# Optimization experiments

Measured on AMD Instinct MI355X. Metric: run time of the kernel, lower is better.

## Reference

```python
import jax, jax.numpy as jnp
import numpy as np

# dims
B, N, C_A, C_S, C_Z = 2, 8192, 128, 384, 16
H, D = 4, 32            # n_heads, head_dim (H*D == C_A)
NQ, NK = 32, 128        # local window: queries / keys
NB = 3                  # n_blocks
W = N // NQ             # number of query windows
HID = 2 * C_A           # transition expansion (n=2)


def _ln(x, eps=1e-5):
    # LayerNorm without affine params
    m = jnp.mean(x, axis=-1, keepdims=True)
    v = jnp.var(x, axis=-1, keepdims=True)
    return (x - m) * jax.lax.rsqrt(v + eps)


def setup_inputs() -> dict:
    key = jax.random.key(0)
    ks = iter(jax.random.split(key, 40))
    def rn(shape, scale=1.0):
        return jax.random.normal(next(ks), shape, dtype=jnp.float32) * jnp.float32(scale)
    inp = {
        'q': rn((B, N, C_A)),
        's': rn((B, N, C_S)),
        'p': rn((B, W, NQ, NK, C_Z)),
        # AttentionPairBias (AF3 Alg 24) params, stacked over blocks
        'adaln_scale_w': rn((NB, C_S, C_A), C_S ** -0.5),
        'adaln_scale_b': jnp.zeros((NB, C_A), jnp.float32),
        'adaln_shift_w': rn((NB, C_S, C_A), C_S ** -0.5),
        'wq': rn((NB, C_A, H * D), C_A ** -0.5),
        'bq': jnp.zeros((NB, H * D), jnp.float32),
        'wk': rn((NB, C_A, H * D), C_A ** -0.5),
        'wv': rn((NB, C_A, H * D), C_A ** -0.5),
        'lnz_w': jnp.ones((NB, C_Z), jnp.float32),
        'lnz_b': jnp.zeros((NB, C_Z), jnp.float32),
        'wb_pair': rn((NB, C_Z, H), C_Z ** -0.5),
        'wg': rn((NB, C_A, H * D), C_A ** -0.5),
        'wo': rn((NB, H * D, C_A), (H * D) ** -0.5),
        'sgate_w': rn((NB, C_S, C_A), C_S ** -0.5),
        'sgate_b': jnp.full((NB, C_A), -2.0, jnp.float32),
        # ConditionedTransitionBlock (AF3 Alg 25) params
        't_scale_w': rn((NB, C_S, C_A), C_S ** -0.5),
        't_scale_b': jnp.zeros((NB, C_A), jnp.float32),
        't_shift_w': rn((NB, C_S, C_A), C_S ** -0.5),
        't_wa': rn((NB, C_A, HID), C_A ** -0.5),
        't_wb': rn((NB, C_A, HID), C_A ** -0.5),
        't_wo': rn((NB, HID, C_A), HID ** -0.5),
        't_sgate_w': rn((NB, C_S, C_A), C_S ** -0.5),
        't_sgate_b': jnp.full((NB, C_A), -2.0, jnp.float32),
    }
    return inp


def reference(q, s, p,
              adaln_scale_w, adaln_scale_b, adaln_shift_w,
              wq, bq, wk, wv, lnz_w, lnz_b, wb_pair, wg, wo, sgate_w, sgate_b,
              t_scale_w, t_scale_b, t_shift_w, t_wa, t_wb, t_wo, t_sgate_w, t_sgate_b):
    a = q
    s_ln = _ln(s)  # [B, N, C_S], shared across blocks
    # local window key indices: window w covers queries [w*NQ, (w+1)*NQ), keys
    # are a centered NK-wide window -> offsets in [-(NK-NQ)//2, ...)
    off = (NK - NQ) // 2
    idx = jnp.arange(W)[:, None] * NQ - off + jnp.arange(NK)[None, :]  # [W, NK]
    valid = (idx >= 0) & (idx < N)
    idx_c = jnp.clip(idx, 0, N - 1)
    inv_sqrt_d = jnp.float32(1.0 / np.sqrt(D))
    NEG = jnp.float32(-1e9)

    for i in range(NB):
        # ---- AttentionPairBias (AdaLN-conditioned, pair-biased, gated) ----
        a_ln = _ln(a)
        a_ln = jax.nn.sigmoid(s_ln @ adaln_scale_w[i] + adaln_scale_b[i]) * a_ln \
               + s_ln @ adaln_shift_w[i]
        qh = (a_ln @ wq[i] + bq[i]).reshape(B, N, H, D)
        kh = (a_ln @ wk[i]).reshape(B, N, H, D)
        vh = (a_ln @ wv[i]).reshape(B, N, H, D)
        g = jax.nn.sigmoid(a_ln @ wg[i]).reshape(B, N, H, D)
        # pair bias from z: LN + linear to heads -> [B, W, NQ, NK, H]
        bias = (_ln(p) * lnz_w[i] + lnz_b[i]) @ wb_pair[i]
        qw = qh.reshape(B, W, NQ, H, D)
        kw = kh[:, idx_c]  # [B, W, NK, H, D]
        vw = vh[:, idx_c]
        logits = jnp.einsum('bwqhd,bwkhd->bwqkh', qw, kw) * inv_sqrt_d + bias
        logits = jnp.where(valid[None, :, None, :, None], logits, NEG)
        attn = jax.nn.softmax(logits, axis=3)
        ow = jnp.einsum('bwqkh,bwkhd->bwqhd', attn, vw)
        o = (g * ow.reshape(B, N, H, D)).reshape(B, N, H * D)
        attn_out = (o @ wo[i]) * jax.nn.sigmoid(s_ln @ sgate_w[i] + sgate_b[i])
        # ---- ConditionedTransitionBlock (SwiGLU, sigmoid-gated) ----
        t_ln = _ln(a)
        t_ln = jax.nn.sigmoid(s_ln @ t_scale_w[i] + t_scale_b[i]) * t_ln \
               + s_ln @ t_shift_w[i]
        hidden = jax.nn.silu(t_ln @ t_wa[i]) * (t_ln @ t_wb[i])
        trans_out = (hidden @ t_wo[i]) * jax.nn.sigmoid(s_ln @ t_sgate_w[i] + t_sgate_b[i])
        # AF3 Alg 23: a <- b + ConditionedTransitionBlock(a, s)
        a = attn_out + trans_out
    return a
```

## Files before the change

kernel.cpp:

```cpp
#include <hip/hip_runtime.h>
#include <hip/hip_bf16.h>
#include <cstddef>
#include <cstdint>

#define BB   2
#define NN   8192
#define CA   128
#define CS   384
#define CZ   16
#define HH   4
#define DD   32
#define NQW  32
#define NKW  128
#define NBLK 3
#define WW   256
#define MR   (BB*NN)
#define HIDN 256

typedef unsigned short u16;
typedef __attribute__((ext_vector_type(8))) short short8;
typedef __attribute__((ext_vector_type(4))) float floatx4;

__device__ __forceinline__ float sigmoidf_(float x) { return 1.f / (1.f + __expf(-x)); }

__device__ __forceinline__ u16 f2bf(float x) {
  unsigned u = __float_as_uint(x);
  unsigned r = (u + 0x7fffu + ((u >> 16) & 1u)) >> 16;
  return (u16)r;
}
__device__ __forceinline__ float bf2f(u16 u) {
  return __uint_as_float(((unsigned)u) << 16);
}

__global__ __launch_bounds__(256) void ln_s_kernel(const float* __restrict__ s,
                                                   u16* __restrict__ s_ln_bf) {
  int row  = blockIdx.x * 4 + (threadIdx.x >> 6);
  int lane = threadIdx.x & 63;
  const float* sr = s + (size_t)row * CS;
  float x[6];
  float sum = 0.f, sq = 0.f;
#pragma unroll
  for (int t = 0; t < 6; ++t) { x[t] = sr[lane + 64*t]; sum += x[t]; sq += x[t]*x[t]; }
#pragma unroll
  for (int off = 32; off; off >>= 1) { sum += __shfl_down(sum, off); sq += __shfl_down(sq, off); }
  sum = __shfl(sum, 0); sq = __shfl(sq, 0);
  float mean = sum * (1.f/CS);
  float var  = sq  * (1.f/CS) - mean*mean;
  float rstd = rsqrtf(var + 1e-5f);
  u16* orow = s_ln_bf + (size_t)row * CS;
#pragma unroll
  for (int t = 0; t < 6; ++t) orow[lane + 64*t] = f2bf((x[t]-mean)*rstd);
}

__global__ __launch_bounds__(256) void modln_kernel(const float* __restrict__ a,
                                                    const u16* __restrict__ sp0,
                                                    const u16* __restrict__ sp1,
                                                    const u16* __restrict__ sp3,
                                                    const u16* __restrict__ sp4,
                                                    u16* __restrict__ amod,
                                                    u16* __restrict__ tmod) {
  int row  = blockIdx.x * 4 + (threadIdx.x >> 6);
  int lane = threadIdx.x & 63;
  const float* ar = a + (size_t)row * CA;
  float x0 = ar[lane], x1 = ar[lane + 64];
  float sum = x0 + x1, sq = x0*x0 + x1*x1;
#pragma unroll
  for (int off = 32; off; off >>= 1) { sum += __shfl_down(sum, off); sq += __shfl_down(sq, off); }
  sum = __shfl(sum, 0); sq = __shfl(sq, 0);
  float mean = sum * (1.f/CA);
  float var  = sq  * (1.f/CA) - mean*mean;
  float rstd = rsqrtf(var + 1e-5f);
  float n0 = (x0-mean)*rstd, n1 = (x1-mean)*rstd;
  size_t i0 = (size_t)row * CA + lane;
  amod[i0]      = f2bf(bf2f(sp0[i0])     *n0 + bf2f(sp1[i0]));
  amod[i0 + 64] = f2bf(bf2f(sp0[i0 + 64])*n1 + bf2f(sp1[i0 + 64]));
  tmod[i0]      = f2bf(bf2f(sp3[i0])     *n0 + bf2f(sp4[i0]));
  tmod[i0 + 64] = f2bf(bf2f(sp3[i0 + 64])*n1 + bf2f(sp4[i0 + 64]));
}

struct TJob { const float* src; u16* dst; int K; int N; };
struct TJobs { TJob j[42]; };

__global__ __launch_bounds__(256) void transpose_bf16(TJobs jobs) {
  TJob jb = jobs.j[blockIdx.z];
  int tk = blockIdx.x * 32, tn = blockIdx.y * 32;
  if (tk >= jb.K || tn >= jb.N) return;
  __shared__ float tile[32][33];
  int tx = threadIdx.x & 31;
  int ty = threadIdx.x >> 5;
#pragma unroll
  for (int r = ty; r < 32; r += 8) tile[r][tx] = jb.src[(size_t)(tk + r) * jb.N + tn + tx];
  __syncthreads();
#pragma unroll
  for (int r = ty; r < 32; r += 8)
    jb.dst[(size_t)(tn + r) * jb.K + tk + tx] = f2bf(tile[tx][r]);
}

struct GemmJob {
  const u16* A;
  const u16* Bt;
  const u16* Bt2;
  const float* bias;
  u16* outbf;
  int K;
  int ostride;
  int mode;
  int pad;
};
struct GemmJobs { GemmJob j[18]; };

#define CH_STRIDE 1032

template <bool DUAL>
__global__ __launch_bounds__(256) void gemm_mfma(GemmJobs jobs) {
  GemmJob jb = jobs.j[blockIdx.z];
  const int bm = blockIdx.y * 128, bn = blockIdx.x * 128;
  const int K = jb.K;

  __shared__ u16 As[4 * CH_STRIDE];
  __shared__ u16 Bs[4 * CH_STRIDE];
  __shared__ u16 Bs2[DUAL ? 4 * CH_STRIDE : 8];

  const int tid  = threadIdx.x;
  const int lane = tid & 63;
  const int wave = tid >> 6;
  const int wr = wave >> 1, wc = wave & 1;
  const int l15 = lane & 15, quad = lane >> 4;

  floatx4 acc[4][4] = {};
  floatx4 acc2[DUAL ? 4 : 1][DUAL ? 4 : 1] = {};

  for (int k0 = 0; k0 < K; k0 += 32) {
    __syncthreads();
#pragma unroll
    for (int h = 0; h < 2; ++h) {
      int f = tid + 256 * h;
      int m = f >> 2, c = f & 3;
      uint4 av = *(const uint4*)(jb.A + (size_t)(bm + m) * K + k0 + c * 8);
      *(uint4*)(As + c * CH_STRIDE + m * 8) = av;
      uint4 bv = *(const uint4*)(jb.Bt + (size_t)(bn + m) * K + k0 + c * 8);
      *(uint4*)(Bs + c * CH_STRIDE + m * 8) = bv;
      if constexpr (DUAL) {
        uint4 bv2 = *(const uint4*)(jb.Bt2 + (size_t)(bn + m) * K + k0 + c * 8);
        *(uint4*)(Bs2 + c * CH_STRIDE + m * 8) = bv2;
      }
    }
    __syncthreads();

    short8 a_frag[4], b_frag[4];
#pragma unroll
    for (int mt = 0; mt < 4; ++mt)
      a_frag[mt] = *(const short8*)(As + quad * CH_STRIDE + (wr * 64 + mt * 16 + l15) * 8);
#pragma unroll
    for (int nt = 0; nt < 4; ++nt)
      b_frag[nt] = *(const short8*)(Bs + quad * CH_STRIDE + (wc * 64 + nt * 16 + l15) * 8);
#pragma unroll
    for (int mt = 0; mt < 4; ++mt)
#pragma unroll
      for (int nt = 0; nt < 4; ++nt)
        acc[mt][nt] = __builtin_amdgcn_mfma_f32_16x16x32_bf16(a_frag[mt], b_frag[nt], acc[mt][nt], 0, 0, 0);
    if constexpr (DUAL) {
      short8 b2_frag[4];
#pragma unroll
      for (int nt = 0; nt < 4; ++nt)
        b2_frag[nt] = *(const short8*)(Bs2 + quad * CH_STRIDE + (wc * 64 + nt * 16 + l15) * 8);
#pragma unroll
      for (int mt = 0; mt < 4; ++mt)
#pragma unroll
        for (int nt = 0; nt < 4; ++nt)
          acc2[mt][nt] = __builtin_amdgcn_mfma_f32_16x16x32_bf16(a_frag[mt], b2_frag[nt], acc2[mt][nt], 0, 0, 0);
    }
  }

#pragma unroll
  for (int mt = 0; mt < 4; ++mt) {
#pragma unroll
    for (int nt = 0; nt < 4; ++nt) {
      int n = bn + wc * 64 + nt * 16 + l15;
      int mbase = bm + wr * 64 + mt * 16 + quad * 4;
      floatx4 v = acc[mt][nt];
      if constexpr (DUAL) {
        floatx4 v2 = acc2[mt][nt];
#pragma unroll
        for (int r = 0; r < 4; ++r) {
          size_t idx = (size_t)(mbase + r) * jb.ostride + n;
          float x1 = v[r];
          jb.outbf[idx] = f2bf(x1 * sigmoidf_(x1) * v2[r]);
        }
      } else if (jb.mode == 5) {
        int bidx = mbase >> 13;
        int tok  = mbase & (NN - 1);
        ushort4 o;
        o.x = f2bf(v[0]); o.y = f2bf(v[1]); o.z = f2bf(v[2]); o.w = f2bf(v[3]);
        *(ushort4*)(jb.outbf + (size_t)(bidx * CA + n) * NN + tok) = o;
      } else {
        float bias = jb.bias ? jb.bias[n] : 0.f;
#pragma unroll
        for (int r = 0; r < 4; ++r) {
          size_t idx = (size_t)(mbase + r) * jb.ostride + n;
          float x = v[r] + bias;
          jb.outbf[idx] = f2bf(jb.mode == 1 ? sigmoidf_(x) : x);
        }
      }
    }
  }
}

__global__ __launch_bounds__(256) void combo_kernel(const u16* __restrict__ O,
                                                    const u16* __restrict__ HID,
                                                    const u16* __restrict__ woT,
                                                    const u16* __restrict__ twoT,
                                                    const u16* __restrict__ g1,
                                                    const u16* __restrict__ g2,
                                                    float* __restrict__ outp) {
  const int bm = blockIdx.y * 128;
  __shared__ u16 As[4 * CH_STRIDE];
  __shared__ u16 Bs[4 * CH_STRIDE];
  const int tid  = threadIdx.x;
  const int lane = tid & 63;
  const int wave = tid >> 6;
  const int wr = wave >> 1, wc = wave & 1;
  const int l15 = lane & 15, quad = lane >> 4;

  floatx4 acc1[4][4] = {};
  floatx4 acc2[4][4] = {};

  for (int k0 = 0; k0 < CA; k0 += 32) {
    __syncthreads();
#pragma unroll
    for (int h = 0; h < 2; ++h) {
      int f = tid + 256 * h;
      int m = f >> 2, c = f & 3;
      *(uint4*)(As + c * CH_STRIDE + m * 8) = *(const uint4*)(O + (size_t)(bm + m) * CA + k0 + c * 8);
      *(uint4*)(Bs + c * CH_STRIDE + m * 8) = *(const uint4*)(woT + (size_t)m * CA + k0 + c * 8);
    }
    __syncthreads();
    short8 a_frag[4], b_frag[4];
#pragma unroll
    for (int mt = 0; mt < 4; ++mt)
      a_frag[mt] = *(const short8*)(As + quad * CH_STRIDE + (wr * 64 + mt * 16 + l15) * 8);
#pragma unroll
    for (int nt = 0; nt < 4; ++nt)
      b_frag[nt] = *(const short8*)(Bs + quad * CH_STRIDE + (wc * 64 + nt * 16 + l15) * 8);
#pragma unroll
    for (int mt = 0; mt < 4; ++mt)
#pragma unroll
      for (int nt = 0; nt < 4; ++nt)
        acc1[mt][nt] = __builtin_amdgcn_mfma_f32_16x16x32_bf16(a_frag[mt], b_frag[nt], acc1[mt][nt], 0, 0, 0);
  }
  for (int k0 = 0; k0 < HIDN; k0 += 32) {
    __syncthreads();
#pragma unroll
    for (int h = 0; h < 2; ++h) {
      int f = tid + 256 * h;
      int m = f >> 2, c = f & 3;
      *(uint4*)(As + c * CH_STRIDE + m * 8) = *(const uint4*)(HID + (size_t)(bm + m) * HIDN + k0 + c * 8);
      *(uint4*)(Bs + c * CH_STRIDE + m * 8) = *(const uint4*)(twoT + (size_t)m * HIDN + k0 + c * 8);
    }
    __syncthreads();
    short8 a_frag[4], b_frag[4];
#pragma unroll
    for (int mt = 0; mt < 4; ++mt)
      a_frag[mt] = *(const short8*)(As + quad * CH_STRIDE + (wr * 64 + mt * 16 + l15) * 8);
#pragma unroll
    for (int nt = 0; nt < 4; ++nt)
      b_frag[nt] = *(const short8*)(Bs + quad * CH_STRIDE + (wc * 64 + nt * 16 + l15) * 8);
#pragma unroll
    for (int mt = 0; mt < 4; ++mt)
#pragma unroll
      for (int nt = 0; nt < 4; ++nt)
        acc2[mt][nt] = __builtin_amdgcn_mfma_f32_16x16x32_bf16(a_frag[mt], b_frag[nt], acc2[mt][nt], 0, 0, 0);
  }

#pragma unroll
  for (int mt = 0; mt < 4; ++mt) {
#pragma unroll
    for (int nt = 0; nt < 4; ++nt) {
      int n = wc * 64 + nt * 16 + l15;
      int mbase = bm + wr * 64 + mt * 16 + quad * 4;
#pragma unroll
      for (int r = 0; r < 4; ++r) {
        size_t idx = (size_t)(mbase + r) * CA + n;
        outp[idx] = acc1[mt][nt][r] * bf2f(g1[idx]) + acc2[mt][nt][r] * bf2f(g2[idx]);
      }
    }
  }
}

__global__ __launch_bounds__(256) void bias3_kernel(const float* __restrict__ p,
                                                    const float* __restrict__ lnz_w,
                                                    const float* __restrict__ lnz_b,
                                                    const float* __restrict__ wb,
                                                    u16* __restrict__ biasT) {
  const int kc = blockIdx.x, w = blockIdx.y, b = blockIdx.z;
  __shared__ float effW[12][16];
  __shared__ float effb[12];
  const int t = threadIdx.x;
  if (t < 192) {
    int i = t >> 6, rem = t & 63, z = rem >> 2, hh = rem & 3;
    effW[i*4 + hh][z] = lnz_w[i*CZ + z] * wb[(i*CZ + z)*HH + hh];
  }
  if (t < 12) {
    int i = t >> 2, hh = t & 3;
    float acc = 0.f;
    for (int z = 0; z < 16; ++z) acc += lnz_b[i*CZ + z] * wb[(i*CZ + z)*HH + hh];
    effb[t] = acc;
  }
  __syncthreads();

  const int kk = t & 31, qg = (t >> 5) * 4;
  const int k = kc * 32 + kk;
  u16 out4[12][4];
#pragma unroll
  for (int r = 0; r < 4; ++r) {
    int qq = qg + r;
    const float4* pr = (const float4*)(p + (size_t)(((b * WW + w) * NQW + qq) * NKW + k) * 16);
    float4 p0 = pr[0], p1 = pr[1], p2 = pr[2], p3 = pr[3];
    float x[16] = {p0.x,p0.y,p0.z,p0.w, p1.x,p1.y,p1.z,p1.w,
                   p2.x,p2.y,p2.z,p2.w, p3.x,p3.y,p3.z,p3.w};
    float sum = 0.f, sq = 0.f;
#pragma unroll
    for (int z = 0; z < 16; ++z) { sum += x[z]; sq += x[z]*x[z]; }
    float mean = sum * (1.f/16.f);
    float var  = sq  * (1.f/16.f) - mean*mean;
    float rstd = rsqrtf(var + 1e-5f);
#pragma unroll
    for (int ih = 0; ih < 12; ++ih) {
      float acc = effb[ih];
#pragma unroll
      for (int z = 0; z < 16; ++z) acc += (x[z]-mean)*rstd * effW[ih][z];
      out4[ih][r] = f2bf(acc);
    }
  }
#pragma unroll
  for (int ih = 0; ih < 12; ++ih) {
    int i = ih >> 2, hh = ih & 3;
    u16* dst = biasT + ((((size_t)i * BB + b) * WW + w) * HH + hh) * 4096 + (size_t)k * 32 + qg;
    ushort4 uv; uv.x = out4[ih][0]; uv.y = out4[ih][1]; uv.z = out4[ih][2]; uv.w = out4[ih][3];
    *(ushort4*)dst = uv;
  }
}

__global__ __launch_bounds__(64) void attn_mfma(const u16* __restrict__ Qb,
                                                const u16* __restrict__ Kb,
                                                const u16* __restrict__ Vtb,
                                                const u16* __restrict__ Gb,
                                                const u16* __restrict__ biasT,
                                                u16* __restrict__ Ob) {
  const int w = blockIdx.x, h = blockIdx.y, b = blockIdx.z;
  __shared__ u16 Pt[128 * 36];
  __shared__ float inv_s[32];
  const int lane = threadIdx.x;
  const int l15 = lane & 15, quad = lane >> 4;
  const int tok0 = w * NQW - 48;

  short8 qf[2];
#pragma unroll
  for (int mt = 0; mt < 2; ++mt) {
    int qq = w * NQW + mt * 16 + l15;
    qf[mt] = *(const short8*)(Qb + (size_t)(b * NN + qq) * CA + h * DD + quad * 8);
  }
  floatx4 lg[2][8] = {};
#pragma unroll
  for (int nt = 0; nt < 8; ++nt) {
    int tk = tok0 + nt * 16 + l15;
    int tc = min(max(tk, 0), NN - 1);
    short8 kf = *(const short8*)(Kb + (size_t)(b * NN + tc) * CA + h * DD + quad * 8);
#pragma unroll
    for (int mt = 0; mt < 2; ++mt)
      lg[mt][nt] = __builtin_amdgcn_mfma_f32_16x16x32_bf16(qf[mt], kf, lg[mt][nt], 0, 0, 0);
  }

  const float scale = 0.17677669529663687f;
  const u16* bb = biasT + ((((size_t)b * WW + w) * HH + h) << 12);
  float mrow[2][4];
#pragma unroll
  for (int mt = 0; mt < 2; ++mt)
#pragma unroll
    for (int r = 0; r < 4; ++r) mrow[mt][r] = -3.0e38f;
#pragma unroll
  for (int nt = 0; nt < 8; ++nt) {
    int tk = tok0 + nt * 16 + l15;
    bool valid = (tk >= 0) && (tk < NN);
#pragma unroll
    for (int mt = 0; mt < 2; ++mt) {
      ushort4 bv = *(const ushort4*)(bb + (nt * 16 + l15) * 32 + mt * 16 + quad * 4);
      float bvf[4] = {bf2f(bv.x), bf2f(bv.y), bf2f(bv.z), bf2f(bv.w)};
#pragma unroll
      for (int r = 0; r < 4; ++r) {
        float l = valid ? (lg[mt][nt][r] * scale + bvf[r]) : -1e9f;
        lg[mt][nt][r] = l;
        mrow[mt][r] = fmaxf(mrow[mt][r], l);
      }
    }
  }
#pragma unroll
  for (int mt = 0; mt < 2; ++mt)
#pragma unroll
    for (int r = 0; r < 4; ++r) {
      float m = mrow[mt][r];
      m = fmaxf(m, __shfl_xor(m, 1));
      m = fmaxf(m, __shfl_xor(m, 2));
      m = fmaxf(m, __shfl_xor(m, 4));
      m = fmaxf(m, __shfl_xor(m, 8));
      mrow[mt][r] = m;
    }

  float srow[2][4] = {};
#pragma unroll
  for (int nt = 0; nt < 8; ++nt)
#pragma unroll
    for (int mt = 0; mt < 2; ++mt) {
      u16 pv[4];
#pragma unroll
      for (int r = 0; r < 4; ++r) {
        float e = __expf(lg[mt][nt][r] - mrow[mt][r]);
        srow[mt][r] += e;
        pv[r] = f2bf(e);
      }
      ushort4 uv; uv.x = pv[0]; uv.y = pv[1]; uv.z = pv[2]; uv.w = pv[3];
      *(ushort4*)(Pt + (nt * 16 + l15) * 36 + mt * 16 + quad * 4) = uv;
    }
#pragma unroll
  for (int mt = 0; mt < 2; ++mt)
#pragma unroll
    for (int r = 0; r < 4; ++r) {
      float ssum = srow[mt][r];
      ssum += __shfl_xor(ssum, 1);
      ssum += __shfl_xor(ssum, 2);
      ssum += __shfl_xor(ssum, 4);
      ssum += __shfl_xor(ssum, 8);
      if (l15 == 0) inv_s[mt * 16 + quad * 4 + r] = 1.f / ssum;
    }
  __syncthreads();

  floatx4 oacc[2][2] = {};
#pragma unroll
  for (int ks = 0; ks < 4; ++ks) {
    short8 pf[2];
#pragma unroll
    for (int ntq = 0; ntq < 2; ++ntq)
#pragma unroll
      for (int j = 0; j < 8; ++j)
        pf[ntq][j] = (short)Pt[(ks * 32 + quad * 8 + j) * 36 + ntq * 16 + l15];
    int tb = tok0 + ks * 32 + quad * 8;
    tb = min(max(tb, 0), NN - 8);
#pragma unroll
    for (int mtd = 0; mtd < 2; ++mtd) {
      short8 vf = *(const short8*)(Vtb + (size_t)(b * CA + h * DD + mtd * 16 + l15) * NN + tb);
#pragma unroll
      for (int ntq = 0; ntq < 2; ++ntq)
        oacc[mtd][ntq] = __builtin_amdgcn_mfma_f32_16x16x32_bf16(vf, pf[ntq], oacc[mtd][ntq], 0, 0, 0);
    }
  }

#pragma unroll
  for (int mtd = 0; mtd < 2; ++mtd)
#pragma unroll
    for (int ntq = 0; ntq < 2; ++ntq) {
      int qq = ntq * 16 + l15;
      float inv = inv_s[qq];
      int tok = w * NQW + qq;
      size_t base = (size_t)(b * NN + tok) * CA + h * DD + mtd * 16 + quad * 4;
      ushort4 gv = *(const ushort4*)(Gb + base);
      floatx4 v = oacc[mtd][ntq];
      ushort4 o;
      o.x = f2bf(bf2f(gv.x) * v[0] * inv);
      o.y = f2bf(bf2f(gv.y) * v[1] * inv);
      o.z = f2bf(bf2f(gv.z) * v[2] * inv);
      o.w = f2bf(bf2f(gv.w) * v[3] * inv);
      *(ushort4*)(Ob + base) = o;
    }
}

extern "C" void kernel_launch(void* const* d_in, const int* in_sizes, int n_in,
                              void* d_out, int out_size, void* d_ws, size_t ws_size,
                              hipStream_t stream) {
  const float* q             = (const float*)d_in[0];
  const float* s             = (const float*)d_in[1];
  const float* p             = (const float*)d_in[2];
  const float* adaln_scale_w = (const float*)d_in[3];
  const float* adaln_scale_b = (const float*)d_in[4];
  const float* adaln_shift_w = (const float*)d_in[5];
  const float* wq            = (const float*)d_in[6];
  const float* bq            = (const float*)d_in[7];
  const float* wk            = (const float*)d_in[8];
  const float* wv            = (const float*)d_in[9];
  const float* lnz_w         = (const float*)d_in[10];
  const float* lnz_b         = (const float*)d_in[11];
  const float* wb_pair       = (const float*)d_in[12];
  const float* wg            = (const float*)d_in[13];
  const float* wo            = (const float*)d_in[14];
  const float* sgate_w       = (const float*)d_in[15];
  const float* sgate_b       = (const float*)d_in[16];
  const float* t_scale_w     = (const float*)d_in[17];
  const float* t_scale_b     = (const float*)d_in[18];
  const float* t_shift_w     = (const float*)d_in[19];
  const float* t_wa          = (const float*)d_in[20];
  const float* t_wb          = (const float*)d_in[21];
  const float* t_wo          = (const float*)d_in[22];
  const float* t_sgate_w     = (const float*)d_in[23];
  const float* t_sgate_b     = (const float*)d_in[24];
  float* out = (float*)d_out;

  const size_t MC = (size_t)MR * CA;
  float* fws   = (float*)d_ws;
  float* abuf0 = fws;
  float* abuf1 = abuf0 + MC;
  u16* uws     = (u16*)(abuf1 + MC);
  u16* s_ln_bf = uws;
  u16* SP      = s_ln_bf + (size_t)MR * CS;
  u16* amod    = SP + 18*MC;
  u16* tmod    = amod + MC;
  u16* Qb      = tmod + MC;
  u16* Kb      = Qb + MC;
  u16* Vtb     = Kb + MC;
  u16* Gb      = Vtb + MC;
  u16* Ob      = Gb + MC;
  u16* HIDb    = Ob + MC;
  u16* biasT   = HIDb + 2*MC;
  u16* wbuf    = biasT + (size_t)3*BB*WW*HH*NQW*NKW;

  const size_t WBLK = 6*(size_t)CA*CS + 5*(size_t)CA*CA + 3*(size_t)CA*HIDN;
  const size_t o_ascale = 0;
  const size_t o_ashift = o_ascale + (size_t)CA*CS;
  const size_t o_sgate  = o_ashift + (size_t)CA*CS;
  const size_t o_tscale = o_sgate  + (size_t)CA*CS;
  const size_t o_tshift = o_tscale + (size_t)CA*CS;
  const size_t o_tsgate = o_tshift + (size_t)CA*CS;
  const size_t o_wq     = o_tsgate + (size_t)CA*CS;
  const size_t o_wk     = o_wq + (size_t)CA*CA;
  const size_t o_wv     = o_wk + (size_t)CA*CA;
  const size_t o_wg     = o_wv + (size_t)CA*CA;
  const size_t o_wo     = o_wg + (size_t)CA*CA;
  const size_t o_twa    = o_wo + (size_t)CA*CA;
  const size_t o_twb    = o_twa + (size_t)HIDN*CA;
  const size_t o_two    = o_twb + (size_t)HIDN*CA;

  ln_s_kernel<<<MR/4, 256, 0, stream>>>(s, s_ln_bf);

  TJobs tj;
  for (int i = 0; i < NBLK; ++i) {
    u16* wb0 = wbuf + (size_t)i * WBLK;
    int b14 = i * 14;
    tj.j[b14+0]  = TJob{adaln_scale_w + (size_t)i*CS*CA, wb0 + o_ascale, CS, CA};
    tj.j[b14+1]  = TJob{adaln_shift_w + (size_t)i*CS*CA, wb0 + o_ashift, CS, CA};
    tj.j[b14+2]  = TJob{sgate_w       + (size_t)i*CS*CA, wb0 + o_sgate,  CS, CA};
    tj.j[b14+3]  = TJob{t_scale_w     + (size_t)i*CS*CA, wb0 + o_tscale, CS, CA};
    tj.j[b14+4]  = TJob{t_shift_w     + (size_t)i*CS*CA, wb0 + o_tshift, CS, CA};
    tj.j[b14+5]  = TJob{t_sgate_w     + (size_t)i*CS*CA, wb0 + o_tsgate, CS, CA};
    tj.j[b14+6]  = TJob{wq   + (size_t)i*CA*CA,   wb0 + o_wq,  CA, CA};
    tj.j[b14+7]  = TJob{wk   + (size_t)i*CA*CA,   wb0 + o_wk,  CA, CA};
    tj.j[b14+8]  = TJob{wv   + (size_t)i*CA*CA,   wb0 + o_wv,  CA, CA};
    tj.j[b14+9]  = TJob{wg   + (size_t)i*CA*CA,   wb0 + o_wg,  CA, CA};
    tj.j[b14+10] = TJob{wo   + (size_t)i*CA*CA,   wb0 + o_wo,  CA, CA};
    tj.j[b14+11] = TJob{t_wa + (size_t)i*CA*HIDN, wb0 + o_twa, CA, HIDN};
    tj.j[b14+12] = TJob{t_wb + (size_t)i*CA*HIDN, wb0 + o_twb, CA, HIDN};
    tj.j[b14+13] = TJob{t_wo + (size_t)i*HIDN*CA, wb0 + o_two, HIDN, CA};
  }
  transpose_bf16<<<dim3(12, 8, 42), 256, 0, stream>>>(tj);

  bias3_kernel<<<dim3(4, WW, BB), 256, 0, stream>>>(p, lnz_w, lnz_b, wb_pair, biasT);

  {
    GemmJobs js = {};
    for (int i = 0; i < NBLK; ++i) {
      u16* wb0 = wbuf + (size_t)i * WBLK;
      js.j[i*6+0] = GemmJob{s_ln_bf, wb0 + o_ascale, nullptr, adaln_scale_b + i*CA, SP + (i*6+0)*MC, CS, CA, 1, 0};
      js.j[i*6+1] = GemmJob{s_ln_bf, wb0 + o_ashift, nullptr, nullptr,              SP + (i*6+1)*MC, CS, CA, 0, 0};
      js.j[i*6+2] = GemmJob{s_ln_bf, wb0 + o_sgate,  nullptr, sgate_b   + i*CA,     SP + (i*6+2)*MC, CS, CA, 1, 0};
      js.j[i*6+3] = GemmJob{s_ln_bf, wb0 + o_tscale, nullptr, t_scale_b + i*CA,     SP + (i*6+3)*MC, CS, CA, 1, 0};
      js.j[i*6+4] = GemmJob{s_ln_bf, wb0 + o_tshift, nullptr, nullptr,              SP + (i*6+4)*MC, CS, CA, 0, 0};
      js.j[i*6+5] = GemmJob{s_ln_bf, wb0 + o_tsgate, nullptr, t_sgate_b + i*CA,     SP + (i*6+5)*MC, CS, CA, 1, 0};
    }
    gemm_mfma<false><<<dim3(1, MR/128, 18), 256, 0, stream>>>(js);
  }

  for (int i = 0; i < NBLK; ++i) {
    const float* a_in = (i == 0) ? q : (i == 1 ? abuf0 : abuf1);
    float* a_out = (i == 2) ? out : (i == 0 ? abuf0 : abuf1);
    u16* wb0 = wbuf + (size_t)i * WBLK;

    modln_kernel<<<MR/4, 256, 0, stream>>>(a_in, SP + (i*6+0)*MC, SP + (i*6+1)*MC,
                                           SP + (i*6+3)*MC, SP + (i*6+4)*MC, amod, tmod);

    GemmJobs jq = {};
    jq.j[0] = GemmJob{amod, wb0 + o_wq, nullptr, bq + i*CA, Qb,  CA, CA, 0, 0};
    jq.j[1] = GemmJob{amod, wb0 + o_wk, nullptr, nullptr,   Kb,  CA, CA, 0, 0};
    jq.j[2] = GemmJob{amod, wb0 + o_wv, nullptr, nullptr,   Vtb, CA, CA, 5, 0};
    jq.j[3] = GemmJob{amod, wb0 + o_wg, nullptr, nullptr,   Gb,  CA, CA, 1, 0};
    gemm_mfma<false><<<dim3(1, MR/128, 4), 256, 0, stream>>>(jq);

    GemmJobs jh = {};
    jh.j[0] = GemmJob{tmod, wb0 + o_twa, wb0 + o_twb, nullptr, HIDb, CA, HIDN, 4, 0};
    gemm_mfma<true><<<dim3(2, MR/128, 1), 256, 0, stream>>>(jh);

    attn_mfma<<<dim3(WW, HH, BB), 64, 0, stream>>>(
        Qb, Kb, Vtb, Gb, biasT + (size_t)i * BB*WW*HH*4096, Ob);

    combo_kernel<<<dim3(1, MR/128), 256, 0, stream>>>(
        Ob, HIDb, wb0 + o_wo, wb0 + o_two,
        SP + (i*6+2)*MC, SP + (i*6+5)*MC, a_out);
  }
}
```

Baseline: 558.0 us.

## Double-buffer GEMM tiles via direct global-to-LDS loads and halve M tile

The GEMM and combo kernels now stage A/B tiles with global_load_lds straight into a double-buffered LDS layout, so the next K-slice loads while MFMAs run on the current one. The M tile shrinks from 128 to 64 rows, doubling the grid for more occupancy and better CU fill on these small-K GEMMs. The combo kernel prefetches across its two GEMM phases. Risks: no explicit wait on the async LDS loads beyond __syncthreads, LDS bank conflicts from the unpadded layout, and more redundant B-tile traffic with smaller M tiles.

```diff
diff --git a/kernel.cpp b/kernel.cpp
--- a/kernel.cpp
+++ b/kernel.cpp
@@ -32,6 +32,12 @@
   return __uint_as_float(((unsigned)u) << 16);
 }
 
+__device__ __forceinline__ void gload16(const u16* g, u16* l) {
+  __builtin_amdgcn_global_load_lds(
+      (const __attribute__((address_space(1))) unsigned int*)g,
+      (__attribute__((address_space(3))) unsigned int*)l, 16, 0, 0);
+}
+
 __global__ __launch_bounds__(256) void ln_s_kernel(const float* __restrict__ s,
                                                    u16* __restrict__ s_ln_bf) {
   int row  = blockIdx.x * 4 + (threadIdx.x >> 6);
@@ -109,17 +115,15 @@
 };
 struct GemmJobs { GemmJob j[18]; };
 
-#define CH_STRIDE 1032
-
 template <bool DUAL>
 __global__ __launch_bounds__(256) void gemm_mfma(GemmJobs jobs) {
   GemmJob jb = jobs.j[blockIdx.z];
-  const int bm = blockIdx.y * 128, bn = blockIdx.x * 128;
+  const int bm = blockIdx.y * 64, bn = blockIdx.x * 128;
   const int K = jb.K;
 
-  __shared__ u16 As[4 * CH_STRIDE];
-  __shared__ u16 Bs[4 * CH_STRIDE];
-  __shared__ u16 Bs2[DUAL ? 4 * CH_STRIDE : 8];
+  __shared__ u16 As[2][2048];
+  __shared__ u16 Bs[2][4096];
+  __shared__ u16 Bs2[DUAL ? 2 : 1][DUAL ? 4096 : 8];
 
   const int tid  = threadIdx.x;
   const int lane = tid & 63;
@@ -127,35 +131,40 @@
   const int wr = wave >> 1, wc = wave & 1;
   const int l15 = lane & 15, quad = lane >> 4;
 
-  floatx4 acc[4][4] = {};
-  floatx4 acc2[DUAL ? 4 : 1][DUAL ? 4 : 1] = {};
-
+  floatx4 acc[2][4] = {};
+  floatx4 acc2[DUAL ? 2 : 1][DUAL ? 4 : 1] = {};
+
+  const u16* Ab   = jb.A  + ((size_t)bm + lane) * K + wave * 8;
+  const u16* Bb0  = jb.Bt + ((size_t)bn + lane) * K + wave * 8;
+  const u16* Bb1  = jb.Bt + ((size_t)bn + 64 + lane) * K + wave * 8;
+  const u16* B2b0 = DUAL ? (jb.Bt2 + ((size_t)bn + lane) * K + wave * 8) : nullptr;
+  const u16* B2b1 = DUAL ? (jb.Bt2 + ((size_t)bn + 64 + lane) * K + wave * 8) : nullptr;
+
+  auto stage = [&](int k0, int pb) {
+    gload16(Ab  + k0, As[pb] + wave * 512);
+    gload16(Bb0 + k0, Bs[pb] + wave * 1024);
+    gload16(Bb1 + k0, Bs[pb] + wave * 1024 + 512);
+    if constexpr (DUAL) {
+      gload16(B2b0 + k0, Bs2[pb] + wave * 1024);
+      gload16(B2b1 + k0, Bs2[pb] + wave * 1024 + 512);
+    }
+  };
+
+  stage(0, 0);
+  __syncthreads();
+  int cur = 0;
   for (int k0 = 0; k0 < K; k0 += 32) {
-    __syncthreads();
-#pragma unroll
-    for (int h = 0; h < 2; ++h) {
-      int f = tid + 256 * h;
-      int m = f >> 2, c = f & 3;
-      uint4 av = *(const uint4*)(jb.A + (size_t)(bm + m) * K + k0 + c * 8);
-      *(uint4*)(As + c * CH_STRIDE + m * 8) = av;
-      uint4 bv = *(const uint4*)(jb.Bt + (size_t)(bn + m) * K + k0 + c * 8);
-      *(uint4*)(Bs + c * CH_STRIDE + m * 8) = bv;
-      if constexpr (DUAL) {
-        uint4 bv2 = *(const uint4*)(jb.Bt2 + (size_t)(bn + m) * K + k0 + c * 8);
-        *(uint4*)(Bs2 + c * CH_STRIDE + m * 8) = bv2;
-      }
-    }
-    __syncthreads();
-
-    short8 a_frag[4], b_frag[4];
-#pragma unroll
-    for (int mt = 0; mt < 4; ++mt)
-      a_frag[mt] = *(const short8*)(As + quad * CH_STRIDE + (wr * 64 + mt * 16 + l15) * 8);
+    if (k0 + 32 < K) stage(k0 + 32, cur ^ 1);
+
+    short8 a_frag[2], b_frag[4];
+#pragma unroll
+    for (int mt = 0; mt < 2; ++mt)
+      a_frag[mt] = *(const short8*)(As[cur] + quad * 512 + (wr * 32 + mt * 16 + l15) * 8);
 #pragma unroll
     for (int nt = 0; nt < 4; ++nt)
-      b_frag[nt] = *(const short8*)(Bs + quad * CH_STRIDE + (wc * 64 + nt * 16 + l15) * 8);
-#pragma unroll
-    for (int mt = 0; mt < 4; ++mt)
+      b_frag[nt] = *(const short8*)(Bs[cur] + quad * 1024 + (wc * 64 + nt * 16 + l15) * 8);
+#pragma unroll
+    for (int mt = 0; mt < 2; ++mt)
 #pragma unroll
       for (int nt = 0; nt < 4; ++nt)
         acc[mt][nt] = __builtin_amdgcn_mfma_f32_16x16x32_bf16(a_frag[mt], b_frag[nt], acc[mt][nt], 0, 0, 0);
@@ -163,21 +172,23 @@
       short8 b2_frag[4];
 #pragma unroll
       for (int nt = 0; nt < 4; ++nt)
-        b2_frag[nt] = *(const short8*)(Bs2 + quad * CH_STRIDE + (wc * 64 + nt * 16 + l15) * 8);
-#pragma unroll
-      for (int mt = 0; mt < 4; ++mt)
+        b2_frag[nt] = *(const short8*)(Bs2[cur] + quad * 1024 + (wc * 64 + nt * 16 + l15) * 8);
+#pragma unroll
+      for (int mt = 0; mt < 2; ++mt)
 #pragma unroll
         for (int nt = 0; nt < 4; ++nt)
           acc2[mt][nt] = __builtin_amdgcn_mfma_f32_16x16x32_bf16(a_frag[mt], b2_frag[nt], acc2[mt][nt], 0, 0, 0);
     }
-  }
-
-#pragma unroll
-  for (int mt = 0; mt < 4; ++mt) {
+    __syncthreads();
+    cur ^= 1;
+  }
+
+#pragma unroll
+  for (int mt = 0; mt < 2; ++mt) {
 #pragma unroll
     for (int nt = 0; nt < 4; ++nt) {
       int n = bn + wc * 64 + nt * 16 + l15;
-      int mbase = bm + wr * 64 + mt * 16 + quad * 4;
+      int mbase = bm + wr * 32 + mt * 16 + quad * 4;
       floatx4 v = acc[mt][nt];
       if constexpr (DUAL) {
         floatx4 v2 = acc2[mt][nt];
@@ -213,71 +224,81 @@
                                                     const u16* __restrict__ g1,
                                                     const u16* __restrict__ g2,
                                                     float* __restrict__ outp) {
-  const int bm = blockIdx.y * 128;
-  __shared__ u16 As[4 * CH_STRIDE];
-  __shared__ u16 Bs[4 * CH_STRIDE];
+  const int bm = blockIdx.y * 64;
+  __shared__ u16 As[2][2048];
+  __shared__ u16 Bs[2][4096];
   const int tid  = threadIdx.x;
   const int lane = tid & 63;
   const int wave = tid >> 6;
   const int wr = wave >> 1, wc = wave & 1;
   const int l15 = lane & 15, quad = lane >> 4;
 
-  floatx4 acc1[4][4] = {};
-  floatx4 acc2[4][4] = {};
-
-  for (int k0 = 0; k0 < CA; k0 += 32) {
-    __syncthreads();
-#pragma unroll
-    for (int h = 0; h < 2; ++h) {
-      int f = tid + 256 * h;
-      int m = f >> 2, c = f & 3;
-      *(uint4*)(As + c * CH_STRIDE + m * 8) = *(const uint4*)(O + (size_t)(bm + m) * CA + k0 + c * 8);
-      *(uint4*)(Bs + c * CH_STRIDE + m * 8) = *(const uint4*)(woT + (size_t)m * CA + k0 + c * 8);
-    }
-    __syncthreads();
-    short8 a_frag[4], b_frag[4];
-#pragma unroll
-    for (int mt = 0; mt < 4; ++mt)
-      a_frag[mt] = *(const short8*)(As + quad * CH_STRIDE + (wr * 64 + mt * 16 + l15) * 8);
+  floatx4 acc1[2][4] = {};
+  floatx4 acc2[2][4] = {};
+
+  const u16* A1  = O   + ((size_t)bm + lane) * CA + wave * 8;
+  const u16* B10 = woT + ((size_t)lane) * CA + wave * 8;
+  const u16* B11 = woT + ((size_t)64 + lane) * CA + wave * 8;
+  const u16* A2  = HID  + ((size_t)bm + lane) * HIDN + wave * 8;
+  const u16* B20 = twoT + ((size_t)lane) * HIDN + wave * 8;
+  const u16* B21 = twoT + ((size_t)64 + lane) * HIDN + wave * 8;
+
+  auto stage1 = [&](int k0, int pb) {
+    gload16(A1  + k0, As[pb] + wave * 512);
+    gload16(B10 + k0, Bs[pb] + wave * 1024);
+    gload16(B11 + k0, Bs[pb] + wave * 1024 + 512);
+  };
+  auto stage2 = [&](int k0, int pb) {
+    gload16(A2  + k0, As[pb] + wave * 512);
+    gload16(B20 + k0, Bs[pb] + wave * 1024);
+    gload16(B21 + k0, Bs[pb] + wave * 1024 + 512);
+  };
+
+  stage1(0, 0);
+  __syncthreads();
+  int cur = 0;
+  for (int t = 0; t < 4; ++t) {
+    if (t < 3) stage1((t + 1) * 32, cur ^ 1);
+    else       stage2(0, cur ^ 1);
+    short8 a_frag[2], b_frag[4];
+#pragma unroll
+    for (int mt = 0; mt < 2; ++mt)
+      a_frag[mt] = *(const short8*)(As[cur] + quad * 512 + (wr * 32 + mt * 16 + l15) * 8);
 #pragma unroll
     for (int nt = 0; nt < 4; ++nt)
-      b_frag[nt] = *(const short8*)(Bs + quad * CH_STRIDE + (wc * 64 + nt * 16 + l15) * 8);
-#pragma unroll
-    for (int mt = 0; mt < 4; ++mt)
+      b_frag[nt] = *(const short8*)(Bs[cur] + quad * 1024 + (wc * 64 + nt * 16 + l15) * 8);
+#pragma unroll
+    for (int mt = 0; mt < 2; ++mt)
 #pragma unroll
       for (int nt = 0; nt < 4; ++nt)
         acc1[mt][nt] = __builtin_amdgcn_mfma_f32_16x16x32_bf16(a_frag[mt], b_frag[nt], acc1[mt][nt], 0, 0, 0);
-  }
-  for (int k0 = 0; k0 < HIDN; k0 += 32) {
     __syncthreads();
-#pragma unroll
-    for (int h = 0; h < 2; ++h) {
-      int f = tid + 256 * h;
-      int m = f >> 2, c = f & 3;
-      *(uint4*)(As + c * CH_STRIDE + m * 8) = *(const uint4*)(HID + (size_t)(bm + m) * HIDN + k0 + c * 8);
-      *(uint4*)(Bs + c * CH_STRIDE + m * 8) = *(const uint4*)(twoT + (size_t)m * HIDN + k0 + c * 8);
-    }
-    __syncthreads();
-    short8 a_frag[4], b_frag[4];
-#pragma unroll
-    for (int mt = 0; mt < 4; ++mt)
-      a_frag[mt] = *(const short8*)(As + quad * CH_STRIDE + (wr * 64 + mt * 16 + l15) * 8);
+    cur ^= 1;
+  }
+  for (int t = 0; t < 8; ++t) {
+    if (t < 7) stage2((t + 1) * 32, cur ^ 1);
+    short8 a_frag[2], b_frag[4];
+#pragma unroll
+    for (int mt = 0; mt < 2; ++mt)
+      a_frag[mt] = *(const short8*)(As[cur] + quad * 512 + (wr * 32 + mt * 16 + l15) * 8);
 #pragma unroll
     for (int nt = 0; nt < 4; ++nt)
-      b_frag[nt] = *(const short8*)(Bs + quad * CH_STRIDE + (wc * 64 + nt * 16 + l15) * 8);
-#pragma unroll
-    for (int mt = 0; mt < 4; ++mt)
+      b_frag[nt] = *(const short8*)(Bs[cur] + quad * 1024 + (wc * 64 + nt * 16 + l15) * 8);
+#pragma unroll
+    for (int mt = 0; mt < 2; ++mt)
 #pragma unroll
       for (int nt = 0; nt < 4; ++nt)
         acc2[mt][nt] = __builtin_amdgcn_mfma_f32_16x16x32_bf16(a_frag[mt], b_frag[nt], acc2[mt][nt], 0, 0, 0);
-  }
-
-#pragma unroll
-  for (int mt = 0; mt < 4; ++mt) {
+    __syncthreads();
+    cur ^= 1;
+  }
+
+#pragma unroll
+  for (int mt = 0; mt < 2; ++mt) {
 #pragma unroll
     for (int nt = 0; nt < 4; ++nt) {
       int n = wc * 64 + nt * 16 + l15;
-      int mbase = bm + wr * 64 + mt * 16 + quad * 4;
+      int mbase = bm + wr * 32 + mt * 16 + quad * 4;
 #pragma unroll
       for (int r = 0; r < 4; ++r) {
         size_t idx = (size_t)(mbase + r) * CA + n;
@@ -573,7 +594,7 @@
       js.j[i*6+4] = GemmJob{s_ln_bf, wb0 + o_tshift, nullptr, nullptr,              SP + (i*6+4)*MC, CS, CA, 0, 0};
       js.j[i*6+5] = GemmJob{s_ln_bf, wb0 + o_tsgate, nullptr, t_sgate_b + i*CA,     SP + (i*6+5)*MC, CS, CA, 1, 0};
     }
-    gemm_mfma<false><<<dim3(1, MR/128, 18), 256, 0, stream>>>(js);
+    gemm_mfma<false><<<dim3(1, MR/64, 18), 256, 0, stream>>>(js);
   }
 
   for (int i = 0; i < NBLK; ++i) {
@@ -589,16 +610,16 @@
     jq.j[1] = GemmJob{amod, wb0 + o_wk, nullptr, nullptr,   Kb,  CA, CA, 0, 0};
     jq.j[2] = GemmJob{amod, wb0 + o_wv, nullptr, nullptr,   Vtb, CA, CA, 5, 0};
     jq.j[3] = GemmJob{amod, wb0 + o_wg, nullptr, nullptr,   Gb,  CA, CA, 1, 0};
-    gemm_mfma<false><<<dim3(1, MR/128, 4), 256, 0, stream>>>(jq);
+    gemm_mfma<false><<<dim3(1, MR/64, 4), 256, 0, stream>>>(jq);
 
     GemmJobs jh = {};
     jh.j[0] = GemmJob{tmod, wb0 + o_twa, wb0 + o_twb, nullptr, HIDb, CA, HIDN, 4, 0};
-    gemm_mfma<true><<<dim3(2, MR/128, 1), 256, 0, stream>>>(jh);
+    gemm_mfma<true><<<dim3(2, MR/64, 1), 256, 0, stream>>>(jh);
 
     attn_mfma<<<dim3(WW, HH, BB), 64, 0, stream>>>(
         Qb, Kb, Vtb, Gb, biasT + (size_t)i * BB*WW*HH*4096, Ob);
 
-    combo_kernel<<<dim3(1, MR/128), 256, 0, stream>>>(
+    combo_kernel<<<dim3(1, MR/64), 256, 0, stream>>>(
         Ob, HIDb, wb0 + o_wo, wb0 + o_two,
         SP + (i*6+2)*MC, SP + (i*6+5)*MC, a_out);
   }
```

Result: slower. 590.6 us (+5.8%).
